# Performance work log

Measured on AMD Instinct MI355X. Metric: run time of the kernel, lower is better.

The kernel has to match this reference:

```python
import jax, jax.numpy as jnp
import numpy as np

EPS = 1e-5
N_HEADS = 12


def _layernorm(x, scale, shift):
    mean = jnp.mean(x, axis=-1, keepdims=True)
    var = jnp.mean((x - mean) ** 2, axis=-1, keepdims=True)
    return scale * (x - mean) / jnp.sqrt(var + EPS) + shift


def setup_inputs() -> dict:
    key = jax.random.key(0)
    ks = jax.random.split(key, 8)
    B, L, D = 4, 1024, 768
    inp = {
        "x": jax.random.normal(ks[0], (B, L, D), jnp.float32),
        "Wq": jax.random.normal(ks[1], (D, D), jnp.float32) * 0.02,
        "Wk": jax.random.normal(ks[2], (D, D), jnp.float32) * 0.02,
        "Wv": jax.random.normal(ks[3], (D, D), jnp.float32) * 0.02,
        "Wo": jax.random.normal(ks[4], (D, D), jnp.float32) * 0.02,
        "bo": jnp.zeros((D,), jnp.float32),
        "scale1": jnp.ones((D,), jnp.float32),
        "shift1": jnp.zeros((D,), jnp.float32),
        "scale2": jnp.ones((D,), jnp.float32),
        "shift2": jnp.zeros((D,), jnp.float32),
        "centers": jax.random.normal(ks[5], (D, D), jnp.float32) * 0.1,  # [num_kernels=D, D]
        "lengthscale": jnp.ones((D,), jnp.float32),
        "Wf": jax.random.normal(ks[6], (D, D), jnp.float32) * 0.02,  # [num_kernels, D]
        "bf": jnp.zeros((D,), jnp.float32),
    }
    return inp


def reference(x, Wq, Wk, Wv, Wo, bo, scale1, shift1, scale2, shift2,
              centers, lengthscale, Wf, bf):
    B, L, D = x.shape
    H = N_HEADS
    hd = D // H

    # --- pre-norm causal MHA + residual ---
    h = _layernorm(x, scale1, shift1)
    q = (h @ Wq).reshape(B, L, H, hd).transpose(0, 2, 1, 3)  # [B,H,L,hd]
    k = (h @ Wk).reshape(B, L, H, hd).transpose(0, 2, 1, 3)
    v = (h @ Wv).reshape(B, L, H, hd).transpose(0, 2, 1, 3)

    scores = jnp.einsum("bhqd,bhkd->bhqk", q, k) / jnp.sqrt(jnp.float32(hd))
    causal = jnp.tril(jnp.ones((L, L), bool))
    scores = jnp.where(causal, scores, -jnp.inf)
    attn = jax.nn.softmax(scores, axis=-1)
    ctx = jnp.einsum("bhqk,bhkd->bhqd", attn, v).transpose(0, 2, 1, 3).reshape(B, L, D)
    x = x + (ctx @ Wo + bo)

    # --- pre-norm RBF-kernel FFN + residual ---
    h = _layernorm(x, scale2, shift2)
    hf = (h / lengthscale).reshape(B * L, D)          # ARD scaling
    cf = centers / lengthscale                        # [K, D]
    sq = (jnp.sum(hf * hf, -1)[:, None]
          + jnp.sum(cf * cf, -1)[None, :]
          - 2.0 * hf @ cf.T)
    K = jnp.exp(-0.5 * jnp.maximum(sq, 0.0))          # [B*L, K]
    ff = (K @ Wf + bf).reshape(B, L, D)
    return x + ff
```

## Files before the change

kernel.cpp:

```cpp
#include <hip/hip_runtime.h>

#define EPS_LN 1e-5f

constexpr int Dm   = 768;
constexpr int Bb   = 4;
constexpr int Ls   = 1024;
constexpr int Hh   = 12;
constexpr int HD   = 64;
constexpr int ROWS = Bb * Ls;
constexpr size_t S = (size_t)ROWS * Dm;
constexpr size_t WSZ = (size_t)Dm * Dm;

typedef __attribute__((ext_vector_type(8))) short bf16x8;
typedef __attribute__((ext_vector_type(4))) float f32x4;
typedef const __attribute__((address_space(1))) unsigned int* gas_p;
typedef __attribute__((address_space(3))) unsigned int* las_p;

__device__ __forceinline__ float u16tof(unsigned short u) {
  union { unsigned int i; float f; } v; v.i = ((unsigned int)u) << 16; return v.f;
}
__device__ __forceinline__ unsigned short f2bf(float f) {
  unsigned int u = __float_as_uint(f);
  u += 0x7fffu + ((u >> 16) & 1u);
  return (unsigned short)(u >> 16);
}
__device__ __forceinline__ void gl_lds16(const unsigned short* g, unsigned short* l) {
  __builtin_amdgcn_global_load_lds((gas_p)g, (las_p)l, 16, 0, 0);
}

__global__ void __launch_bounds__(256) prep_kernel(
    const float* __restrict__ W0, const float* __restrict__ W1,
    const float* __restrict__ W2, const float* __restrict__ W3,
    const float* __restrict__ W4, unsigned short* __restrict__ wtBase,
    const float* __restrict__ centers, const float* __restrict__ ls,
    unsigned short* __restrict__ cb, float* __restrict__ cn,
    const float* __restrict__ x, const float* __restrict__ scale,
    const float* __restrict__ shift, unsigned short* __restrict__ hb)
{
  __shared__ float smem[64 * 65];
  int bx = blockIdx.x, t = threadIdx.x;
  if (bx < 720) {
    int w = bx / 144, rem = bx - w * 144;
    int ky = rem / 12, nx = rem - ky * 12;
    const float* W = w == 0 ? W0 : w == 1 ? W1 : w == 2 ? W2 : w == 3 ? W3 : W4;
    unsigned short* WT = wtBase + (size_t)w * WSZ;
    int k0 = ky * 64, n0 = nx * 64;
    int c = t & 63, r4 = t >> 6;
    #pragma unroll
    for (int p = 0; p < 16; p++) {
      int r = p * 4 + r4;
      smem[r * 65 + c] = W[(size_t)(k0 + r) * Dm + n0 + c];
    }
    __syncthreads();
    #pragma unroll
    for (int p = 0; p < 16; p++) {
      int r = p * 4 + r4;
      WT[(size_t)(n0 + r) * Dm + k0 + c] = f2bf(smem[c * 65 + r]);
    }
  } else if (bx < 1488) {
    int j = bx - 720;
    float s = 0.f;
    #pragma unroll
    for (int i = 0; i < 3; i++) {
      int k = t + 256 * i;
      float c = centers[(size_t)j * Dm + k] / ls[k];
      cb[(size_t)j * Dm + k] = f2bf(c);
      s += c * c;
    }
    smem[t] = s; __syncthreads();
    for (int o = 128; o > 0; o >>= 1) { if (t < o) smem[t] += smem[t + o]; __syncthreads(); }
    if (t == 0) cn[j] = smem[0];
  } else {
    int row = bx - 1488;
    size_t base = (size_t)row * Dm;
    float v0 = x[base + t], v1 = x[base + t + 256], v2 = x[base + t + 512];
    smem[t] = v0 + v1 + v2; __syncthreads();
    for (int o = 128; o > 0; o >>= 1) { if (t < o) smem[t] += smem[t + o]; __syncthreads(); }
    float mean = smem[0] * (1.0f / Dm);
    __syncthreads();
    float d0 = v0 - mean, d1 = v1 - mean, d2 = v2 - mean;
    smem[t] = d0*d0 + d1*d1 + d2*d2; __syncthreads();
    for (int o = 128; o > 0; o >>= 1) { if (t < o) smem[t] += smem[t + o]; __syncthreads(); }
    float rstd = rsqrtf(smem[0] * (1.0f / Dm) + EPS_LN);
    float dd[3] = {d0, d1, d2};
    #pragma unroll
    for (int i = 0; i < 3; i++) {
      int c = t + 256 * i;
      hb[base + c] = f2bf(scale[c] * dd[i] * rstd + shift[c]);
    }
  }
}

__global__ void __launch_bounds__(256) ln2_kernel(
    const float* __restrict__ xin, const float* __restrict__ scale,
    const float* __restrict__ shift, const float* __restrict__ ls,
    unsigned short* __restrict__ o, float* __restrict__ hn)
{
  int row = blockIdx.x, t = threadIdx.x;
  __shared__ float red[256];
  size_t base = (size_t)row * Dm;
  float v0 = xin[base + t], v1 = xin[base + t + 256], v2 = xin[base + t + 512];
  red[t] = v0 + v1 + v2; __syncthreads();
  for (int oo = 128; oo > 0; oo >>= 1) { if (t < oo) red[t] += red[t + oo]; __syncthreads(); }
  float mean = red[0] * (1.0f / Dm);
  __syncthreads();
  float d0 = v0 - mean, d1 = v1 - mean, d2 = v2 - mean;
  red[t] = d0*d0 + d1*d1 + d2*d2; __syncthreads();
  for (int oo = 128; oo > 0; oo >>= 1) { if (t < oo) red[t] += red[t + oo]; __syncthreads(); }
  float rstd = rsqrtf(red[0] * (1.0f / Dm) + EPS_LN);
  float dd[3] = {d0, d1, d2};
  float hsum = 0.f;
  #pragma unroll
  for (int i = 0; i < 3; i++) {
    int c = t + 256 * i;
    float hv = (scale[c] * dd[i] * rstd + shift[c]) / ls[c];
    o[base + c] = f2bf(hv);
    hsum += hv * hv;
  }
  __syncthreads();
  red[t] = hsum; __syncthreads();
  for (int o2 = 128; o2 > 0; o2 >>= 1) { if (t < o2) red[t] += red[t + o2]; __syncthreads(); }
  if (t == 0) hn[row] = red[0];
}

__global__ void __launch_bounds__(256) gemm_qkv(
    const unsigned short* __restrict__ Abf,
    const unsigned short* __restrict__ wqT,
    const unsigned short* __restrict__ wkT,
    const unsigned short* __restrict__ wvT,
    unsigned short* __restrict__ qb,
    unsigned short* __restrict__ kb,
    unsigned short* __restrict__ vbt)
{
  int m0 = blockIdx.y * 64, n0 = blockIdx.x * 64;
  __shared__ unsigned short sm[4096 + 3 * 4096];
  int tid = threadIdx.x;
  int lane = tid & 63, wave = tid >> 6;
  int quad = lane >> 4, l15 = lane & 15;
  int wr = (wave >> 1) << 5, wc = (wave & 1) << 5;

  f32x4 acc[3][2][2];
  #pragma unroll
  for (int w = 0; w < 3; w++)
    #pragma unroll
    for (int i = 0; i < 2; i++)
      #pragma unroll
      for (int j = 0; j < 2; j++) acc[w][i][j] = (f32x4){0.f, 0.f, 0.f, 0.f};

  const unsigned short* gA = Abf + (size_t)(m0 + (tid >> 2)) * Dm + ((tid & 3) << 3);
  size_t bOff = (size_t)(n0 + (tid >> 2)) * Dm + ((tid & 3) << 3);
  const unsigned short* gB[3] = { wqT + bOff, wkT + bOff, wvT + bOff };

  union Frag { bf16x8 v; ushort4 h[2]; };

  for (int k0 = 0; k0 < Dm; k0 += 64) {
    gl_lds16(gA + k0,      &sm[tid * 8]);
    gl_lds16(gA + k0 + 32, &sm[2048 + tid * 8]);
    #pragma unroll
    for (int w = 0; w < 3; w++) {
      gl_lds16(gB[w] + k0,      &sm[4096 + w * 4096 + tid * 8]);
      gl_lds16(gB[w] + k0 + 32, &sm[4096 + w * 4096 + 2048 + tid * 8]);
    }
    __syncthreads();
    Frag af[2][2];
    #pragma unroll
    for (int kc = 0; kc < 2; kc++)
      #pragma unroll
      for (int mi = 0; mi < 2; mi++)
        af[kc][mi].v = *(const bf16x8*)&sm[kc * 2048 + (wr + mi * 16 + l15) * 32 + quad * 8];
    #pragma unroll
    for (int w = 0; w < 3; w++)
      #pragma unroll
      for (int kc = 0; kc < 2; kc++)
        #pragma unroll
        for (int ni = 0; ni < 2; ni++) {
          Frag bf;
          bf.v = *(const bf16x8*)&sm[4096 + w * 4096 + kc * 2048 + (wc + ni * 16 + l15) * 32 + quad * 8];
          #pragma unroll
          for (int mi = 0; mi < 2; mi++)
            acc[w][mi][ni] = __builtin_amdgcn_mfma_f32_16x16x32_bf16(
                af[kc][mi].v, bf.v, acc[w][mi][ni], 0, 0, 0);
        }
    __syncthreads();
  }

  #pragma unroll
  for (int w = 0; w < 2; w++) {
    unsigned short* ob = w ? kb : qb;
    #pragma unroll
    for (int mi = 0; mi < 2; mi++)
      #pragma unroll
      for (int ni = 0; ni < 2; ni++)
        #pragma unroll
        for (int rg = 0; rg < 4; rg++) {
          int gr = m0 + wr + mi * 16 + quad * 4 + rg;
          int gc = n0 + wc + ni * 16 + l15;
          ob[(size_t)gr * Dm + gc] = f2bf(acc[w][mi][ni][rg]);
        }
  }
  #pragma unroll
  for (int mi = 0; mi < 2; mi++)
    #pragma unroll
    for (int ni = 0; ni < 2; ni++)
      #pragma unroll
      for (int rg = 0; rg < 4; rg++) {
        int rl = wr + mi * 16 + quad * 4 + rg;
        int cl = wc + ni * 16 + l15;
        sm[cl * 72 + rl] = f2bf(acc[2][mi][ni][rg]);
      }
  __syncthreads();
  {
    int d = tid >> 2, c0 = (tid & 3) * 16;
    int b_ = m0 >> 10, keybase = m0 & 1023;
    unsigned short* dst = vbt + ((size_t)((blockIdx.x * 4 + b_) * 64 + d)) * 1024 + keybase + c0;
    #pragma unroll
    for (int i = 0; i < 16; i += 4)
      *(ushort4*)(dst + i) = *(const ushort4*)&sm[d * 72 + c0 + i];
  }
}

template<int MODE>
__global__ void __launch_bounds__(256) gemm64(
    const unsigned short* __restrict__ Abf,
    const unsigned short* __restrict__ BT,
    unsigned short* __restrict__ o0,
    float* __restrict__ outF,
    const float* __restrict__ residF,
    const float* __restrict__ biasF,
    const float* __restrict__ hn,
    const float* __restrict__ cn)
{
  int m0 = blockIdx.y * 64, n0 = blockIdx.x * 64;
  __shared__ unsigned short Asm[2][2048];
  __shared__ unsigned short Bsm[2][2048];
  int tid = threadIdx.x;
  int lane = tid & 63, wave = tid >> 6;
  int quad = lane >> 4, l15 = lane & 15;
  int wr = (wave >> 1) << 5, wc = (wave & 1) << 5;

  f32x4 acc[2][2];
  #pragma unroll
  for (int i = 0; i < 2; i++)
    #pragma unroll
    for (int j = 0; j < 2; j++) acc[i][j] = (f32x4){0.f, 0.f, 0.f, 0.f};

  const unsigned short* gA = Abf + (size_t)(m0 + (tid >> 2)) * Dm + ((tid & 3) << 3);
  const unsigned short* gB = BT  + (size_t)(n0 + (tid >> 2)) * Dm + ((tid & 3) << 3);

  union Frag { bf16x8 v; ushort4 h[2]; };

  for (int k0 = 0; k0 < Dm; k0 += 64) {
    gl_lds16(gA + k0,      &Asm[0][tid * 8]);
    gl_lds16(gA + k0 + 32, &Asm[1][tid * 8]);
    gl_lds16(gB + k0,      &Bsm[0][tid * 8]);
    gl_lds16(gB + k0 + 32, &Bsm[1][tid * 8]);
    __syncthreads();
    #pragma unroll
    for (int kc = 0; kc < 2; kc++) {
      Frag af[2], bfb[2];
      #pragma unroll
      for (int i = 0; i < 2; i++) {
        af[i].v  = *(const bf16x8*)&Asm[kc][(wr + i * 16 + l15) * 32 + quad * 8];
        bfb[i].v = *(const bf16x8*)&Bsm[kc][(wc + i * 16 + l15) * 32 + quad * 8];
      }
      #pragma unroll
      for (int mi = 0; mi < 2; mi++)
        #pragma unroll
        for (int ni = 0; ni < 2; ni++)
          acc[mi][ni] = __builtin_amdgcn_mfma_f32_16x16x32_bf16(
              af[mi].v, bfb[ni].v, acc[mi][ni], 0, 0, 0);
    }
    __syncthreads();
  }

  #pragma unroll
  for (int mi = 0; mi < 2; mi++)
    #pragma unroll
    for (int ni = 0; ni < 2; ni++)
      #pragma unroll
      for (int rg = 0; rg < 4; rg++) {
        int gr = m0 + wr + mi * 16 + quad * 4 + rg;
        int gc = n0 + wc + ni * 16 + l15;
        size_t idx = (size_t)gr * Dm + gc;
        float v = acc[mi][ni][rg];
        if (MODE == 2) {
          float sq = fmaxf(hn[gr] + cn[gc] - 2.0f * v, 0.f);
          o0[idx] = f2bf(__expf(-0.5f * sq));
        } else {
          outF[idx] = residF[idx] + v + biasF[gc];
        }
      }
}

__global__ void __launch_bounds__(256) attn_flash(
    const unsigned short* __restrict__ q,
    const unsigned short* __restrict__ k,
    const unsigned short* __restrict__ vbt,
    unsigned short* __restrict__ ctx)
{
  int bx = blockIdx.x;
  int qt = (bx & 1) ? (15 - (bx >> 1)) : (bx >> 1);
  int h  = blockIdx.y;
  int b  = blockIdx.z;
  int tid = threadIdx.x;
  int lane = tid & 63, wave = tid >> 6;
  int quad = lane >> 4, l15 = lane & 15;

  __shared__ unsigned short Ks[2][2048];
  __shared__ unsigned short Vt[2][2048];
  __shared__ unsigned short QP[4608];

  size_t baseQK = (size_t)(b * Ls) * Dm + h * HD;
  const unsigned short* gVt = vbt + (size_t)((h * 4 + b) * 64 + (tid >> 2)) * 1024 + ((tid & 3) << 3);

  {
    const unsigned short* gQ = q + baseQK + (size_t)(qt * 64 + (tid >> 2)) * Dm + ((tid & 3) << 3);
    gl_lds16(gQ,      &QP[tid * 8]);
    gl_lds16(gQ + 32, &QP[2048 + tid * 8]);
  }
  __syncthreads();

  union Frag { bf16x8 v; ushort4 h[2]; };
  Frag afq[2];
  #pragma unroll
  for (int kc = 0; kc < 2; kc++)
    afq[kc].v = *(const bf16x8*)&QP[kc * 2048 + (wave * 16 + l15) * 32 + quad * 8];

  f32x4 O[4];
  #pragma unroll
  for (int nj = 0; nj < 4; nj++) O[nj] = (f32x4){0.f, 0.f, 0.f, 0.f};
  float lsum[4] = {0.f, 0.f, 0.f, 0.f};

  const unsigned short* gK = k + baseQK + (size_t)(tid >> 2) * Dm + ((tid & 3) << 3);

  for (int kt = 0; kt <= qt; kt++) {
    gl_lds16(gK + (size_t)(kt * 64) * Dm,      &Ks[0][tid * 8]);
    gl_lds16(gK + (size_t)(kt * 64) * Dm + 32, &Ks[1][tid * 8]);
    gl_lds16(gVt + kt * 64,      &Vt[0][tid * 8]);
    gl_lds16(gVt + kt * 64 + 32, &Vt[1][tid * 8]);
    __syncthreads();

    f32x4 sacc[4];
    #pragma unroll
    for (int ni = 0; ni < 4; ni++) {
      sacc[ni] = (f32x4){0.f, 0.f, 0.f, 0.f};
      #pragma unroll
      for (int kc = 0; kc < 2; kc++) {
        Frag bk;
        bk.v = *(const bf16x8*)&Ks[kc][((ni & 1) * 32 + (ni >> 1) * 16 + l15) * 32 + quad * 8];
        sacc[ni] = __builtin_amdgcn_mfma_f32_16x16x32_bf16(afq[kc].v, bk.v, sacc[ni], 0, 0, 0);
      }
    }

    #pragma unroll
    for (int ni = 0; ni < 4; ni++) {
      sacc[ni] = (f32x4){0.f, 0.f, 0.f, 0.f};
      #pragma unroll
      for (int kc = 0; kc < 2; kc++) {
        Frag bk;
        bk.v = *(const bf16x8*)&Ks[kc][(ni * 16 + l15) * 32 + quad * 8];
        sacc[ni] = __builtin_amdgcn_mfma_f32_16x16x32_bf16(afq[kc].v, bk.v, sacc[ni], 0, 0, 0);
      }
    }

    if (kt == qt) {
      #pragma unroll
      for (int ni = 0; ni < 4; ni++)
        #pragma unroll
        for (int rg = 0; rg < 4; rg++) {
          int rowl = wave * 16 + quad * 4 + rg;
          int coll = ni * 16 + l15;
          if (coll > rowl) sacc[ni][rg] = -1e30f;
        }
    }

    unsigned short (*Ps)[72] = (unsigned short(*)[72])QP;
    #pragma unroll
    for (int ni = 0; ni < 4; ni++)
      #pragma unroll
      for (int rg = 0; rg < 4; rg++) {
        float p = __expf(sacc[ni][rg] * 0.125f);
        lsum[rg] += p;
        Ps[wave * 16 + quad * 4 + rg][ni * 16 + l15] = f2bf(p);
      }

    Frag ap[2];
    #pragma unroll
    for (int kc = 0; kc < 2; kc++)
      ap[kc].v = *(const bf16x8*)&Ps[wave * 16 + l15][kc * 32 + quad * 8];

    #pragma unroll
    for (int nj = 0; nj < 4; nj++)
      #pragma unroll
      for (int kc = 0; kc < 2; kc++) {
        Frag bv;
        bv.v = *(const bf16x8*)&Vt[kc][(nj * 16 + l15) * 32 + quad * 8];
        O[nj] = __builtin_amdgcn_mfma_f32_16x16x32_bf16(ap[kc].v, bv.v, O[nj], 0, 0, 0);
      }
    __syncthreads();
  }

  float linv[4];
  #pragma unroll
  for (int rg = 0; rg < 4; rg++) {
    float l = lsum[rg];
    #pragma unroll
    for (int m = 1; m < 16; m <<= 1) l += __shfl_xor(l, m, 16);
    linv[rg] = 1.0f / l;
  }
  #pragma unroll
  for (int nj = 0; nj < 4; nj++)
    #pragma unroll
    for (int rg = 0; rg < 4; rg++) {
      int row = qt * 64 + wave * 16 + quad * 4 + rg;
      int col = nj * 16 + l15;
      ctx[baseQK + (size_t)row * Dm + col] = f2bf(O[nj][rg] * linv[rg]);
    }
}

extern "C" void kernel_launch(void* const* d_in, const int* in_sizes, int n_in,
                              void* d_out, int out_size, void* d_ws, size_t ws_size,
                              hipStream_t stream)
{
  const float* x      = (const float*)d_in[0];
  const float* Wq     = (const float*)d_in[1];
  const float* Wk     = (const float*)d_in[2];
  const float* Wv     = (const float*)d_in[3];
  const float* Wo     = (const float*)d_in[4];
  const float* bo     = (const float*)d_in[5];
  const float* scale1 = (const float*)d_in[6];
  const float* shift1 = (const float*)d_in[7];
  const float* scale2 = (const float*)d_in[8];
  const float* shift2 = (const float*)d_in[9];
  const float* centers= (const float*)d_in[10];
  const float* lsp    = (const float*)d_in[11];
  const float* Wf     = (const float*)d_in[12];
  const float* bfv    = (const float*)d_in[13];
  float* out = (float*)d_out;

  unsigned short* wsu = (unsigned short*)d_ws;
  unsigned short* wqT = wsu;
  unsigned short* wkT = wsu + WSZ;
  unsigned short* wvT = wsu + 2 * WSZ;
  unsigned short* woT = wsu + 3 * WSZ;
  unsigned short* wfT = wsu + 4 * WSZ;
  unsigned short* cb  = wsu + 5 * WSZ;
  unsigned short* bufA = wsu + 6 * WSZ;
  unsigned short* bufB = bufA + S;
  unsigned short* hb  = bufA;
  unsigned short* qb  = bufB;
  unsigned short* kb  = bufB + S;
  unsigned short* vbt = bufB + 2 * S;
  unsigned short* ctx = bufA;
  float* x1f          = (float*)bufB;
  unsigned short* hf  = bufB + 2 * S;
  unsigned short* Km  = bufA;
  float* hn = (float*)(bufB + 3 * S);
  float* cn = hn + ROWS;

  dim3 gg(Dm / 64, ROWS / 64);

  prep_kernel<<<5584, 256, 0, stream>>>(Wq, Wk, Wv, Wo, Wf, wsu,
                                        centers, lsp, cb, cn,
                                        x, scale1, shift1, hb);
  gemm_qkv<<<dim3(12, 64), 256, 0, stream>>>(hb, wqT, wkT, wvT, qb, kb, vbt);
  attn_flash<<<dim3(Ls / 64, Hh, Bb), 256, 0, stream>>>(qb, kb, vbt, ctx);
  gemm64<1><<<gg, 256, 0, stream>>>(ctx, woT, nullptr, x1f, x, bo, nullptr, nullptr);
  ln2_kernel<<<ROWS, 256, 0, stream>>>(x1f, scale2, shift2, lsp, hf, hn);
  gemm64<2><<<gg, 256, 0, stream>>>(hf, cb, Km, nullptr, nullptr, nullptr, hn, cn);
  gemm64<3><<<gg, 256, 0, stream>>>(Km, wfT, nullptr, out, x1f, bfv, nullptr, nullptr);
}
```

Before: 197.2 us.

## Enlarge GEMM tiles to 128x128 and attention key tiles to 128

```diff
diff --git a/kernel.cpp b/kernel.cpp
--- a/kernel.cpp
+++ b/kernel.cpp
@@ -16,9 +16,6 @@
 typedef const __attribute__((address_space(1))) unsigned int* gas_p;
 typedef __attribute__((address_space(3))) unsigned int* las_p;
 
-__device__ __forceinline__ float u16tof(unsigned short u) {
-  union { unsigned int i; float f; } v; v.i = ((unsigned int)u) << 16; return v.f;
-}
 __device__ __forceinline__ unsigned short f2bf(float f) {
   unsigned int u = __float_as_uint(f);
   u += 0x7fffu + ((u >> 16) & 1u);
@@ -220,7 +217,7 @@
 }
 
 template<int MODE>
-__global__ void __launch_bounds__(256) gemm64(
+__global__ void __launch_bounds__(256) gemm128(
     const unsigned short* __restrict__ Abf,
     const unsigned short* __restrict__ BT,
     unsigned short* __restrict__ o0,
@@ -230,53 +227,51 @@
     const float* __restrict__ hn,
     const float* __restrict__ cn)
 {
-  int m0 = blockIdx.y * 64, n0 = blockIdx.x * 64;
-  __shared__ unsigned short Asm[2][2048];
-  __shared__ unsigned short Bsm[2][2048];
+  int m0 = blockIdx.y * 128, n0 = blockIdx.x * 128;
+  __shared__ unsigned short Asm[128 * 32];
+  __shared__ unsigned short Bsm[128 * 32];
   int tid = threadIdx.x;
   int lane = tid & 63, wave = tid >> 6;
   int quad = lane >> 4, l15 = lane & 15;
-  int wr = (wave >> 1) << 5, wc = (wave & 1) << 5;
-
-  f32x4 acc[2][2];
-  #pragma unroll
-  for (int i = 0; i < 2; i++)
-    #pragma unroll
-    for (int j = 0; j < 2; j++) acc[i][j] = (f32x4){0.f, 0.f, 0.f, 0.f};
+  int wr = (wave >> 1) << 6, wc = (wave & 1) << 6;
+
+  f32x4 acc[4][4];
+  #pragma unroll
+  for (int i = 0; i < 4; i++)
+    #pragma unroll
+    for (int j = 0; j < 4; j++) acc[i][j] = (f32x4){0.f, 0.f, 0.f, 0.f};
 
   const unsigned short* gA = Abf + (size_t)(m0 + (tid >> 2)) * Dm + ((tid & 3) << 3);
   const unsigned short* gB = BT  + (size_t)(n0 + (tid >> 2)) * Dm + ((tid & 3) << 3);
+  const size_t rowOff = (size_t)64 * Dm;
 
   union Frag { bf16x8 v; ushort4 h[2]; };
 
-  for (int k0 = 0; k0 < Dm; k0 += 64) {
-    gl_lds16(gA + k0,      &Asm[0][tid * 8]);
-    gl_lds16(gA + k0 + 32, &Asm[1][tid * 8]);
-    gl_lds16(gB + k0,      &Bsm[0][tid * 8]);
-    gl_lds16(gB + k0 + 32, &Bsm[1][tid * 8]);
-    __syncthreads();
-    #pragma unroll
-    for (int kc = 0; kc < 2; kc++) {
-      Frag af[2], bfb[2];
-      #pragma unroll
-      for (int i = 0; i < 2; i++) {
-        af[i].v  = *(const bf16x8*)&Asm[kc][(wr + i * 16 + l15) * 32 + quad * 8];
-        bfb[i].v = *(const bf16x8*)&Bsm[kc][(wc + i * 16 + l15) * 32 + quad * 8];
-      }
-      #pragma unroll
-      for (int mi = 0; mi < 2; mi++)
-        #pragma unroll
-        for (int ni = 0; ni < 2; ni++)
-          acc[mi][ni] = __builtin_amdgcn_mfma_f32_16x16x32_bf16(
-              af[mi].v, bfb[ni].v, acc[mi][ni], 0, 0, 0);
-    }
-    __syncthreads();
-  }
-
-  #pragma unroll
-  for (int mi = 0; mi < 2; mi++)
-    #pragma unroll
-    for (int ni = 0; ni < 2; ni++)
+  for (int k0 = 0; k0 < Dm; k0 += 32) {
+    gl_lds16(gA + k0,          &Asm[tid * 8]);
+    gl_lds16(gA + rowOff + k0, &Asm[tid * 8 + 2048]);
+    gl_lds16(gB + k0,          &Bsm[tid * 8]);
+    gl_lds16(gB + rowOff + k0, &Bsm[tid * 8 + 2048]);
+    __syncthreads();
+    Frag af[4], bfb[4];
+    #pragma unroll
+    for (int i = 0; i < 4; i++) {
+      af[i].v  = *(const bf16x8*)&Asm[(wr + i * 16 + l15) * 32 + quad * 8];
+      bfb[i].v = *(const bf16x8*)&Bsm[(wc + i * 16 + l15) * 32 + quad * 8];
+    }
+    #pragma unroll
+    for (int mi = 0; mi < 4; mi++)
+      #pragma unroll
+      for (int ni = 0; ni < 4; ni++)
+        acc[mi][ni] = __builtin_amdgcn_mfma_f32_16x16x32_bf16(
+            af[mi].v, bfb[ni].v, acc[mi][ni], 0, 0, 0);
+    __syncthreads();
+  }
+
+  #pragma unroll
+  for (int mi = 0; mi < 4; mi++)
+    #pragma unroll
+    for (int ni = 0; ni < 4; ni++)
       #pragma unroll
       for (int rg = 0; rg < 4; rg++) {
         int gr = m0 + wr + mi * 16 + quad * 4 + rg;
@@ -306,12 +301,11 @@
   int lane = tid & 63, wave = tid >> 6;
   int quad = lane >> 4, l15 = lane & 15;
 
-  __shared__ unsigned short Ks[2][2048];
-  __shared__ unsigned short Vt[2][2048];
-  __shared__ unsigned short QP[4608];
+  __shared__ unsigned short Ks[2][4096];
+  __shared__ unsigned short Vt[4][2048];
+  __shared__ unsigned short QP[8192];
 
   size_t baseQK = (size_t)(b * Ls) * Dm + h * HD;
-  const unsigned short* gVt = vbt + (size_t)((h * 4 + b) * 64 + (tid >> 2)) * 1024 + ((tid & 3) << 3);
 
   {
     const unsigned short* gQ = q + baseQK + (size_t)(qt * 64 + (tid >> 2)) * Dm + ((tid & 3) << 3);
@@ -331,68 +325,65 @@
   for (int nj = 0; nj < 4; nj++) O[nj] = (f32x4){0.f, 0.f, 0.f, 0.f};
   float lsum[4] = {0.f, 0.f, 0.f, 0.f};
 
-  const unsigned short* gK = k + baseQK + (size_t)(tid >> 2) * Dm + ((tid & 3) << 3);
-
-  for (int kt = 0; kt <= qt; kt++) {
-    gl_lds16(gK + (size_t)(kt * 64) * Dm,      &Ks[0][tid * 8]);
-    gl_lds16(gK + (size_t)(kt * 64) * Dm + 32, &Ks[1][tid * 8]);
-    gl_lds16(gVt + kt * 64,      &Vt[0][tid * 8]);
-    gl_lds16(gVt + kt * 64 + 32, &Vt[1][tid * 8]);
-    __syncthreads();
-
-    f32x4 sacc[4];
-    #pragma unroll
-    for (int ni = 0; ni < 4; ni++) {
-      sacc[ni] = (f32x4){0.f, 0.f, 0.f, 0.f};
+  const unsigned short* gK  = k + baseQK + (size_t)(tid >> 2) * Dm + ((tid & 3) << 3);
+  const unsigned short* gVt = vbt + (size_t)((h * 4 + b) * 64 + (tid >> 2)) * 1024 + ((tid & 3) << 3);
+  const size_t kRow64 = (size_t)64 * Dm;
+
+  int nt2 = (qt >> 1) + 1;
+  int lastTile = qt >> 1;
+
+  for (int kt2 = 0; kt2 < nt2; kt2++) {
+    const unsigned short* gKt = gK + (size_t)(kt2 * 128) * Dm;
+    gl_lds16(gKt,               &Ks[0][tid * 8]);
+    gl_lds16(gKt + kRow64,      &Ks[0][2048 + tid * 8]);
+    gl_lds16(gKt + 32,          &Ks[1][tid * 8]);
+    gl_lds16(gKt + kRow64 + 32, &Ks[1][2048 + tid * 8]);
+    #pragma unroll
+    for (int qr = 0; qr < 4; qr++)
+      gl_lds16(gVt + kt2 * 128 + qr * 32, &Vt[qr][tid * 8]);
+    __syncthreads();
+
+    f32x4 sacc[8];
+    #pragma unroll
+    for (int nk = 0; nk < 8; nk++) {
+      sacc[nk] = (f32x4){0.f, 0.f, 0.f, 0.f};
       #pragma unroll
       for (int kc = 0; kc < 2; kc++) {
         Frag bk;
-        bk.v = *(const bf16x8*)&Ks[kc][((ni & 1) * 32 + (ni >> 1) * 16 + l15) * 32 + quad * 8];
-        sacc[ni] = __builtin_amdgcn_mfma_f32_16x16x32_bf16(afq[kc].v, bk.v, sacc[ni], 0, 0, 0);
+        bk.v = *(const bf16x8*)&Ks[kc][(nk * 16 + l15) * 32 + quad * 8];
+        sacc[nk] = __builtin_amdgcn_mfma_f32_16x16x32_bf16(afq[kc].v, bk.v, sacc[nk], 0, 0, 0);
       }
     }
 
-    #pragma unroll
-    for (int ni = 0; ni < 4; ni++) {
-      sacc[ni] = (f32x4){0.f, 0.f, 0.f, 0.f};
-      #pragma unroll
-      for (int kc = 0; kc < 2; kc++) {
-        Frag bk;
-        bk.v = *(const bf16x8*)&Ks[kc][(ni * 16 + l15) * 32 + quad * 8];
-        sacc[ni] = __builtin_amdgcn_mfma_f32_16x16x32_bf16(afq[kc].v, bk.v, sacc[ni], 0, 0, 0);
-      }
-    }
-
-    if (kt == qt) {
-      #pragma unroll
-      for (int ni = 0; ni < 4; ni++)
+    if (kt2 == lastTile) {
+      #pragma unroll
+      for (int nk = 0; nk < 8; nk++)
         #pragma unroll
         for (int rg = 0; rg < 4; rg++) {
-          int rowl = wave * 16 + quad * 4 + rg;
-          int coll = ni * 16 + l15;
-          if (coll > rowl) sacc[ni][rg] = -1e30f;
+          int rowg = qt * 64 + wave * 16 + quad * 4 + rg;
+          int keyg = kt2 * 128 + nk * 16 + l15;
+          if (keyg > rowg) sacc[nk][rg] = -1e30f;
         }
     }
 
-    unsigned short (*Ps)[72] = (unsigned short(*)[72])QP;
-    #pragma unroll
-    for (int ni = 0; ni < 4; ni++)
+    #pragma unroll
+    for (int nk = 0; nk < 8; nk++)
       #pragma unroll
       for (int rg = 0; rg < 4; rg++) {
-        float p = __expf(sacc[ni][rg] * 0.125f);
+        float p = __expf(sacc[nk][rg] * 0.125f);
         lsum[rg] += p;
-        Ps[wave * 16 + quad * 4 + rg][ni * 16 + l15] = f2bf(p);
+        QP[(nk >> 1) * 2048 + (wave * 16 + quad * 4 + rg) * 32 + (nk & 1) * 16 + l15] = f2bf(p);
       }
 
-    Frag ap[2];
-    #pragma unroll
-    for (int kc = 0; kc < 2; kc++)
-      ap[kc].v = *(const bf16x8*)&Ps[wave * 16 + l15][kc * 32 + quad * 8];
+    Frag ap[4];
+    #pragma unroll
+    for (int kc = 0; kc < 4; kc++)
+      ap[kc].v = *(const bf16x8*)&QP[kc * 2048 + (wave * 16 + l15) * 32 + quad * 8];
 
     #pragma unroll
     for (int nj = 0; nj < 4; nj++)
       #pragma unroll
-      for (int kc = 0; kc < 2; kc++) {
+      for (int kc = 0; kc < 4; kc++) {
         Frag bv;
         bv.v = *(const bf16x8*)&Vt[kc][(nj * 16 + l15) * 32 + quad * 8];
         O[nj] = __builtin_amdgcn_mfma_f32_16x16x32_bf16(ap[kc].v, bv.v, O[nj], 0, 0, 0);
@@ -458,15 +449,15 @@
   float* hn = (float*)(bufB + 3 * S);
   float* cn = hn + ROWS;
 
-  dim3 gg(Dm / 64, ROWS / 64);
+  dim3 g128(Dm / 128, ROWS / 128);
 
   prep_kernel<<<5584, 256, 0, stream>>>(Wq, Wk, Wv, Wo, Wf, wsu,
                                         centers, lsp, cb, cn,
                                         x, scale1, shift1, hb);
   gemm_qkv<<<dim3(12, 64), 256, 0, stream>>>(hb, wqT, wkT, wvT, qb, kb, vbt);
   attn_flash<<<dim3(Ls / 64, Hh, Bb), 256, 0, stream>>>(qb, kb, vbt, ctx);
-  gemm64<1><<<gg, 256, 0, stream>>>(ctx, woT, nullptr, x1f, x, bo, nullptr, nullptr);
+  gemm128<1><<<g128, 256, 0, stream>>>(ctx, woT, nullptr, x1f, x, bo, nullptr, nullptr);
   ln2_kernel<<<ROWS, 256, 0, stream>>>(x1f, scale2, shift2, lsp, hf, hn);
-  gemm64<2><<<gg, 256, 0, stream>>>(hf, cb, Km, nullptr, nullptr, nullptr, hn, cn);
-  gemm64<3><<<gg, 256, 0, stream>>>(Km, wfT, nullptr, out, x1f, bfv, nullptr, nullptr);
-}
+  gemm128<2><<<g128, 256, 0, stream>>>(hf, cb, Km, nullptr, nullptr, nullptr, hn, cn);
+  gemm128<3><<<g128, 256, 0, stream>>>(Km, wfT, nullptr, out, x1f, bfv, nullptr, nullptr);
+}
```

Result: slower. 244.6 us (+24.1%).
